# Optimization experiments

Measured on AMD Instinct MI355X. Metric: run time of the kernel, lower is better.

Reference implementation:

```python
import jax, jax.numpy as jnp
import numpy as np

N = 50000      # nodes
E = 1600000    # edges (before self loops)
F = 128        # input_dim
H = 4          # num_heads
D = 32         # hidden_dim (per head)
B = 16         # graphs in batch
NEG_SLOPE = 0.2  # PyG GATv2Conv default negative_slope


def setup_inputs() -> dict:
    key = jax.random.key(0)
    ks = jax.random.split(key, 8)
    x = jax.random.normal(ks[0], (N, F), dtype=jnp.float32)
    edge_index = jax.random.randint(ks[1], (2, E), 0, N, dtype=jnp.int32)
    batch = jnp.sort(jax.random.randint(ks[2], (N,), 0, B, dtype=jnp.int32))
    s = 0.05
    W_l = jax.random.normal(ks[3], (F, H * D), dtype=jnp.float32) * s
    b_l = jnp.zeros((H * D,), dtype=jnp.float32)
    W_r = jax.random.normal(ks[4], (F, H * D), dtype=jnp.float32) * s
    b_r = jnp.zeros((H * D,), dtype=jnp.float32)
    att = jax.random.normal(ks[5], (H, D), dtype=jnp.float32) * s
    bias = jnp.zeros((H * D,), dtype=jnp.float32)
    return {"x": x, "edge_index": edge_index, "batch": batch,
            "W_l": W_l, "b_l": b_l, "W_r": W_r, "b_r": b_r,
            "att": att, "bias": bias}


def reference(x, edge_index, batch, W_l, b_l, W_r, b_r, att, bias):
    n = x.shape[0]
    # PyG GATv2Conv adds self loops by default
    loops = jnp.arange(n, dtype=edge_index.dtype)
    src = jnp.concatenate([edge_index[0], loops])  # message source j
    dst = jnp.concatenate([edge_index[1], loops])  # message target i

    xl = (x @ W_l + b_l).reshape(n, H, D)  # source transform
    xr = (x @ W_r + b_r).reshape(n, H, D)  # target transform

    # per-edge GATv2 attention logits: a^T LeakyReLU(xl_j + xr_i)
    m = xl[src] + xr[dst]                                   # [E+N, H, D]
    e = jnp.sum(jax.nn.leaky_relu(m, NEG_SLOPE) * att, -1)  # [E+N, H]

    # softmax over incoming edges of each destination node
    e_max = jax.ops.segment_max(e, dst, num_segments=n)
    ex = jnp.exp(e - e_max[dst])
    den = jax.ops.segment_sum(ex, dst, num_segments=n)
    alpha = ex / den[dst]                                   # [E+N, H]

    # weighted scatter-sum aggregation of source features
    out = jax.ops.segment_sum(alpha[..., None] * xl[src], dst, num_segments=n)
    out = out.reshape(n, H * D) + bias                      # concat heads + bias
    out = jax.nn.relu(out)

    # global max pool over nodes of each graph
    pooled = jax.ops.segment_max(out, batch, num_segments=B)
    pooled = jnp.where(jnp.isfinite(pooled), pooled, 0.0)   # guard empty graphs
    return pooled
```

## Files before the change

### kernel.cpp

```cpp
#include <hip/hip_runtime.h>

#define NN 50000
#define NE 1600000
#define FDIM 128
#define CDIM 128
#define NGRAPH 16
#define SLOPE 0.2f
#define CSTRIDE 96
#define BINSH 7
#define NBIN 391
#define EPB 6400
#define NB1 250
#define EPT 25
#define CAP 5120
#define POOL_NODES 64
#define POOL_NB ((NN + POOL_NODES - 1) / POOL_NODES)
#define TNB 782

__device__ __forceinline__ unsigned short f2bf(float f) {
    unsigned u = __float_as_uint(f);
    return (unsigned short)((u + 0x7FFFu + ((u >> 16) & 1u)) >> 16);
}
__device__ __forceinline__ unsigned packbf(float a, float b) {
    return (unsigned)f2bf(a) | ((unsigned)f2bf(b) << 16);
}
#define BFLO(u) __uint_as_float((u) << 16)
#define BFHI(u) __uint_as_float((u) & 0xffff0000u)

typedef __attribute__((ext_vector_type(8))) short short8;
typedef __attribute__((ext_vector_type(4))) float f32x4;
union FragU { uint4 u; short8 s; };

__global__ __launch_bounds__(256) void k_init(float* __restrict__ out,
                                              int* __restrict__ gbin_cnt) {
    int i = blockIdx.x * 256 + threadIdx.x;
    if (i < NGRAPH * CDIM) out[i] = 0.f;
    if (i < NBIN) gbin_cnt[i] = 0;
}

__global__ __launch_bounds__(256) void k_front(
    const float* __restrict__ x,
    const float* __restrict__ Wl, const float* __restrict__ bl,
    const float* __restrict__ Wr, const float* __restrict__ br,
    const int* __restrict__ src, const int* __restrict__ dst,
    int* __restrict__ gbin_cnt, unsigned* __restrict__ gstage,
    unsigned short* __restrict__ xlh, float* __restrict__ xr) {
    __shared__ __align__(16) char shraw[32768];
    const int tid = threadIdx.x;

    if (blockIdx.x < NB1) {
        int* bcnt = (int*)shraw;
        int* boff = bcnt + NBIN;
        int* gb   = boff + NBIN;
        int* sc   = gb + NBIN;
        unsigned* st = (unsigned*)(sc + 256);
        const int t  = tid;
        const int e0 = blockIdx.x * EPB;

        for (int b = t; b < NBIN; b += 256) bcnt[b] = 0;
        __syncthreads();

        unsigned sd[EPT]; int bn[EPT]; int pl[EPT];
#pragma unroll
        for (int k = 0; k < EPT; k++) {
            int e = e0 + k * 256 + t;
            int s = src[e], d = dst[e];
            bn[k] = d >> BINSH;
            sd[k] = (unsigned)s | ((unsigned)(d & 127) << 16)
                                | ((unsigned)bn[k] << 23);
            pl[k] = atomicAdd(&bcnt[bn[k]], 1);
        }
        __syncthreads();

        int c0 = (2*t     < NBIN) ? bcnt[2*t]     : 0;
        int c1 = (2*t + 1 < NBIN) ? bcnt[2*t + 1] : 0;
        int v  = c0 + c1;
        sc[t] = v; __syncthreads();
        for (int off = 1; off < 256; off <<= 1) {
            int add = (t >= off) ? sc[t - off] : 0;
            __syncthreads();
            sc[t] += add;
            __syncthreads();
        }
        int base = sc[t] - v;
        if (2*t     < NBIN) boff[2*t]     = base;
        if (2*t + 1 < NBIN) boff[2*t + 1] = base + c0;
        __syncthreads();

        for (int b = t; b < NBIN; b += 256) {
            int c = bcnt[b];
            gb[b] = (c > 0) ? atomicAdd(&gbin_cnt[b], c) : 0;
        }
#pragma unroll
        for (int k = 0; k < EPT; k++) st[boff[bn[k]] + pl[k]] = sd[k];
        __syncthreads();

        for (int idx = t; idx < EPB; idx += 256) {
            unsigned w = st[idx];
            int b = w >> 23;
            int p = gb[b] + (idx - boff[b]);
            if (p < CAP) gstage[(size_t)b * CAP + p] = w;
        }
    } else {
        uint4* wfrag = (uint4*)shraw;
        const int bid   = blockIdx.x - NB1;
        const int wv    = tid >> 6;
        const int lane  = tid & 63;
        const int quad  = lane >> 4;
        const int col   = lane & 15;
        const int node0 = bid * 64;
        const int nodeA = node0 + wv * 16 + col;
        const bool aval = nodeA < NN;

        FragU afrag[4];
#pragma unroll
        for (int kq = 0; kq < 4; kq++) {
            float4 lo = make_float4(0.f,0.f,0.f,0.f), hi = lo;
            if (aval) {
                const float* ap = &x[(size_t)nodeA * FDIM + kq * 32 + quad * 8];
                lo = *(const float4*)ap;
                hi = *(const float4*)(ap + 4);
            }
            afrag[kq].u.x = packbf(lo.x, lo.y);
            afrag[kq].u.y = packbf(lo.z, lo.w);
            afrag[kq].u.z = packbf(hi.x, hi.y);
            afrag[kq].u.w = packbf(hi.z, hi.w);
        }

        const int myrow0 = node0 + wv * 16 + quad * 4;

        for (int mat = 0; mat < 2; mat++) {
            const float* W  = mat ? Wr : Wl;
            const float* bb = mat ? br : bl;
            __syncthreads();
            for (int i = 0; i < 8; i++) {
                int C = i * 256 + tid;
                int ccol = C & 15, cq = (C >> 4) & 3, ckq = (C >> 6) & 3, cnt_ = C >> 8;
                const float* wp = &W[(size_t)(ckq * 32 + cq * 8) * CDIM + cnt_ * 16 + ccol];
                uint4 u;
                u.x = packbf(wp[0],        wp[CDIM]);
                u.y = packbf(wp[2*CDIM],   wp[3*CDIM]);
                u.z = packbf(wp[4*CDIM],   wp[5*CDIM]);
                u.w = packbf(wp[6*CDIM],   wp[7*CDIM]);
                wfrag[C] = u;
            }
            __syncthreads();

#pragma unroll
            for (int nt = 0; nt < 8; nt++) {
                f32x4 acc = {0.f, 0.f, 0.f, 0.f};
#pragma unroll
                for (int kq = 0; kq < 4; kq++) {
                    FragU bfr;
                    bfr.u = wfrag[(nt * 4 + kq) * 64 + lane];
                    acc = __builtin_amdgcn_mfma_f32_16x16x32_bf16(
                              afrag[kq].s, bfr.s, acc, 0, 0, 0);
                }
                int ch = nt * 16 + col;
                float bv = bb[ch];
                if (mat == 0) {
#pragma unroll
                    for (int r = 0; r < 4; r++) {
                        int node = myrow0 + r;
                        if (node < NN)
                            xlh[(size_t)node * CDIM + ch] = f2bf(acc[r] + bv);
                    }
                } else {
#pragma unroll
                    for (int r = 0; r < 4; r++) {
                        int node = myrow0 + r;
                        if (node < NN)
                            xr[(size_t)node * CDIM + ch] = acc[r] + bv;
                    }
                }
            }
        }
    }
}

__global__ __launch_bounds__(512) void k_csr(
    const int* __restrict__ gbin_cnt, const unsigned* __restrict__ gstage,
    int* __restrict__ cnt, unsigned short* __restrict__ colp) {
    __shared__ int nfill[128];
    __shared__ unsigned short crow[128 * CSTRIDE];
    const int bin = blockIdx.x;
    const int t   = threadIdx.x;
    const int n0  = bin << BINSH;
    const int nb  = min(128, NN - n0);
    const int m   = min(gbin_cnt[bin], CAP);

    if (t < 128) nfill[t] = 0;
    __syncthreads();

    unsigned w[10];
    bool     ok[10];
#pragma unroll
    for (int k = 0; k < 10; k++) {
        int i = k * 512 + t;
        ok[k] = i < m;
        if (ok[k]) w[k] = gstage[(size_t)bin * CAP + i];
    }
#pragma unroll
    for (int k = 0; k < 10; k++) {
        if (ok[k]) {
            int dl = (w[k] >> 16) & 127;
            int p  = atomicAdd(&nfill[dl], 1);
            if (p < CSTRIDE - 1)
                crow[dl * CSTRIDE + p] = (unsigned short)(w[k] & 0xFFFF);
        }
    }
    __syncthreads();

    if (t < nb) {
        int c = min(nfill[t], CSTRIDE - 1);
        crow[t * CSTRIDE + c] = (unsigned short)(n0 + t);
        cnt[n0 + t] = c + 1;
    }
    __syncthreads();

    unsigned* gout = (unsigned*)colp + (size_t)bin * (128 * CSTRIDE / 2);
    const unsigned* cin = (const unsigned*)crow;
    for (int idx = t; idx < 128 * CSTRIDE / 2; idx += 512) gout[idx] = cin[idx];
}

__device__ __forceinline__ void edge_body(
    const unsigned short* __restrict__ xlh, int j, int ch0,
    const float4& rx0, const float4& rx1,
    const float4& p0, const float4& p1,
    const float4& q0, const float4& q1,
    float& s, float* acc) {
    uint4 q = *(const uint4*)&xlh[(size_t)j * CDIM + ch0];
    float4 v0 = make_float4(BFLO(q.x), BFHI(q.x), BFLO(q.y), BFHI(q.y));
    float4 v1 = make_float4(BFLO(q.z), BFHI(q.z), BFLO(q.w), BFHI(q.w));
    float t0, d = 0.f;
    t0 = v0.x + rx0.x; d = fmaf(t0, p0.x, d); d = fmaf(fabsf(t0), q0.x, d);
    t0 = v0.y + rx0.y; d = fmaf(t0, p0.y, d); d = fmaf(fabsf(t0), q0.y, d);
    t0 = v0.z + rx0.z; d = fmaf(t0, p0.z, d); d = fmaf(fabsf(t0), q0.z, d);
    t0 = v0.w + rx0.w; d = fmaf(t0, p0.w, d); d = fmaf(fabsf(t0), q0.w, d);
    t0 = v1.x + rx1.x; d = fmaf(t0, p1.x, d); d = fmaf(fabsf(t0), q1.x, d);
    t0 = v1.y + rx1.y; d = fmaf(t0, p1.y, d); d = fmaf(fabsf(t0), q1.y, d);
    t0 = v1.z + rx1.z; d = fmaf(t0, p1.z, d); d = fmaf(fabsf(t0), q1.z, d);
    t0 = v1.w + rx1.w; d = fmaf(t0, p1.w, d); d = fmaf(fabsf(t0), q1.w, d);
    d += __shfl_xor(d, 1);
    d += __shfl_xor(d, 2);
    float w = __expf(d);
    s += w;
    acc[0] = fmaf(w, v0.x, acc[0]);
    acc[1] = fmaf(w, v0.y, acc[1]);
    acc[2] = fmaf(w, v0.z, acc[2]);
    acc[3] = fmaf(w, v0.w, acc[3]);
    acc[4] = fmaf(w, v1.x, acc[4]);
    acc[5] = fmaf(w, v1.y, acc[5]);
    acc[6] = fmaf(w, v1.z, acc[6]);
    acc[7] = fmaf(w, v1.w, acc[7]);
}

__global__ __launch_bounds__(256) void k_aggregate(
    const unsigned short* __restrict__ xlh, const float* __restrict__ xr,
    const float* __restrict__ att, const float* __restrict__ bias,
    const int* __restrict__ cnt, const unsigned short* __restrict__ colp,
    float* __restrict__ nodeout) {
    const int wave = blockIdx.x * 4 + (threadIdx.x >> 6);
    const int lane = threadIdx.x & 63;
    const int i     = wave;
    const size_t start = (size_t)i * CSTRIDE;
    const int deg   = cnt[i];
    const int grp   = lane >> 4;
    const int ch0   = (lane & 15) * 8;

    int cj0 = (int)colp[start + lane];
    int cj1 = 0;
    if (deg > 64) cj1 = (int)colp[start + 64 + lane];

    const float4 rx0 = *(const float4*)&xr[(size_t)i * CDIM + ch0];
    const float4 rx1 = *(const float4*)&xr[(size_t)i * CDIM + ch0 + 4];
    const float4 aa0 = *(const float4*)&att[ch0];
    const float4 aa1 = *(const float4*)&att[ch0 + 4];
    const float4 p0 = make_float4(0.6f*aa0.x, 0.6f*aa0.y, 0.6f*aa0.z, 0.6f*aa0.w);
    const float4 p1 = make_float4(0.6f*aa1.x, 0.6f*aa1.y, 0.6f*aa1.z, 0.6f*aa1.w);
    const float4 q0 = make_float4(0.4f*aa0.x, 0.4f*aa0.y, 0.4f*aa0.z, 0.4f*aa0.w);
    const float4 q1 = make_float4(0.4f*aa1.x, 0.4f*aa1.y, 0.4f*aa1.z, 0.4f*aa1.w);

    float s = 0.f;
    float acc[8];
#pragma unroll
    for (int k = 0; k < 8; k++) acc[k] = 0.f;

    const int full = deg >> 2;
    const int f0   = full < 16 ? full : 16;
#pragma unroll 2
    for (int t = 0; t < f0; t++) {
        int j = __shfl(cj0, t * 4 + grp);
        edge_body(xlh, j, ch0, rx0, rx1, p0, p1, q0, q1, s, acc);
    }
    for (int t = 16; t < full; t++) {
        int j = __shfl(cj1, t * 4 + grp - 64);
        edge_body(xlh, j, ch0, rx0, rx1, p0, p1, q0, q1, s, acc);
    }
    int e  = full * 4 + grp;
    int jt = (e < 64) ? __shfl(cj0, e) : __shfl(cj1, (e - 64) & 63);
    if (e < deg)
        edge_body(xlh, jt, ch0, rx0, rx1, p0, p1, q0, q1, s, acc);

#pragma unroll
    for (int dist = 16; dist <= 32; dist <<= 1) {
        s += __shfl_xor(s, dist);
#pragma unroll
        for (int k = 0; k < 8; k++) acc[k] += __shfl_xor(acc[k], dist);
    }

    if (grp == 0) {
        float inv = 1.f / s;
        float4 o0, o1;
        const float4 b0 = *(const float4*)&bias[ch0];
        const float4 b1 = *(const float4*)&bias[ch0 + 4];
        o0.x = fmaxf(fmaf(acc[0], inv, b0.x), 0.f);
        o0.y = fmaxf(fmaf(acc[1], inv, b0.y), 0.f);
        o0.z = fmaxf(fmaf(acc[2], inv, b0.z), 0.f);
        o0.w = fmaxf(fmaf(acc[3], inv, b0.w), 0.f);
        o1.x = fmaxf(fmaf(acc[4], inv, b1.x), 0.f);
        o1.y = fmaxf(fmaf(acc[5], inv, b1.y), 0.f);
        o1.z = fmaxf(fmaf(acc[6], inv, b1.z), 0.f);
        o1.w = fmaxf(fmaf(acc[7], inv, b1.w), 0.f);
        float* op = &nodeout[(size_t)i * CDIM + ch0];
        *(float4*)op       = o0;
        *(float4*)(op + 4) = o1;
    }
}

__global__ __launch_bounds__(256) void k_pool(
    const float* __restrict__ nodeout, const int* __restrict__ batch,
    float* __restrict__ out) {
    const int tid  = threadIdx.x;
    const int c4   = (tid & 31) * 4;
    const int nl   = tid >> 5;
    const int base = blockIdx.x * POOL_NODES;
    float4 mx = make_float4(0.f, 0.f, 0.f, 0.f);
    int cur = -1;
#pragma unroll
    for (int k = 0; k < POOL_NODES / 8; k++) {
        int node = base + k * 8 + nl;
        if (node >= NN) break;
        int g = batch[node];
        if (g != cur) {
            if (cur >= 0) {
                int* op = (int*)&out[cur * CDIM + c4];
                if (mx.x > 0.f) atomicMax(op,     __float_as_int(mx.x));
                if (mx.y > 0.f) atomicMax(op + 1, __float_as_int(mx.y));
                if (mx.z > 0.f) atomicMax(op + 2, __float_as_int(mx.z));
                if (mx.w > 0.f) atomicMax(op + 3, __float_as_int(mx.w));
            }
            cur = g;
            mx = make_float4(0.f, 0.f, 0.f, 0.f);
        }
        float4 v = *(const float4*)&nodeout[(size_t)node * CDIM + c4];
        mx.x = fmaxf(mx.x, v.x);
        mx.y = fmaxf(mx.y, v.y);
        mx.z = fmaxf(mx.z, v.z);
        mx.w = fmaxf(mx.w, v.w);
    }
    if (cur >= 0) {
        int* op = (int*)&out[cur * CDIM + c4];
        if (mx.x > 0.f) atomicMax(op,     __float_as_int(mx.x));
        if (mx.y > 0.f) atomicMax(op + 1, __float_as_int(mx.y));
        if (mx.z > 0.f) atomicMax(op + 2, __float_as_int(mx.z));
        if (mx.w > 0.f) atomicMax(op + 3, __float_as_int(mx.w));
    }
}

extern "C" void kernel_launch(void* const* d_in, const int* in_sizes, int n_in,
                              void* d_out, int out_size, void* d_ws, size_t ws_size,
                              hipStream_t stream) {
    const float* x     = (const float*)d_in[0];
    const int*   ei    = (const int*)d_in[1];
    const int*   batch = (const int*)d_in[2];
    const float* Wl    = (const float*)d_in[3];
    const float* bl    = (const float*)d_in[4];
    const float* Wr    = (const float*)d_in[5];
    const float* br    = (const float*)d_in[6];
    const float* att   = (const float*)d_in[7];
    const float* bias  = (const float*)d_in[8];
    float* out = (float*)d_out;

    char* w = (char*)d_ws;
    float*          xr       = (float*)w;          w += (size_t)NN * CDIM * 4;
    float*          nodeout  = (float*)w;          w += (size_t)NN * CDIM * 4;
    unsigned short* xlh      = (unsigned short*)w; w += (size_t)NN * CDIM * 2;
    int*            cnt      = (int*)w;            w += (size_t)NN * 4;
    unsigned short* colp     = (unsigned short*)w; w += (size_t)NBIN * 128 * CSTRIDE * 2;
    unsigned*       gstage   = (unsigned*)w;       w += (size_t)NBIN * CAP * 4;
    int*            gbin_cnt = (int*)w;            w += (size_t)NBIN * 4;

    const int* src = ei;
    const int* dst = ei + NE;

    k_init<<<10, 256, 0, stream>>>(out, gbin_cnt);
    k_front<<<NB1 + TNB, 256, 0, stream>>>(x, Wl, bl, Wr, br,
                                           src, dst, gbin_cnt, gstage, xlh, xr);
    k_csr<<<NBIN, 512, 0, stream>>>(gbin_cnt, gstage, cnt, colp);
    k_aggregate<<<NN / 4, 256, 0, stream>>>(xlh, xr, att, bias,
                                            cnt, colp, nodeout);
    k_pool<<<POOL_NB, 256, 0, stream>>>(nodeout, batch, out);
}
```

Baseline: 233.0 us.

## Use fp16 packed math for edge logits and fuse max-pool into aggregation

Stores both xl and xr as fp16 instead of bf16 and fp32. The per-edge logit is computed with packed half adds, a max-based LeakyReLU and fdot2 dot products, replacing the scalar fp32 FMA chain. The separate pooling kernel and the nodeout buffer are removed: each node's result goes straight into the per-graph output through atomicMax, guarded by a pre-read. This cuts memory traffic and per-edge ALU work, at the cost of fp16 precision loss and more global atomics on the 16x128 output.

```diff
diff --git a/kernel.cpp b/kernel.cpp
--- a/kernel.cpp
+++ b/kernel.cpp
@@ -13,8 +13,6 @@
 #define NB1 250
 #define EPT 25
 #define CAP 5120
-#define POOL_NODES 64
-#define POOL_NB ((NN + POOL_NODES - 1) / POOL_NODES)
 #define TNB 782
 
 __device__ __forceinline__ unsigned short f2bf(float f) {
@@ -24,12 +22,17 @@
 __device__ __forceinline__ unsigned packbf(float a, float b) {
     return (unsigned)f2bf(a) | ((unsigned)f2bf(b) << 16);
 }
-#define BFLO(u) __uint_as_float((u) << 16)
-#define BFHI(u) __uint_as_float((u) & 0xffff0000u)
+__device__ __forceinline__ unsigned short f2h(float f) {
+    union { _Float16 h; unsigned short u; } c;
+    c.h = (_Float16)f;
+    return c.u;
+}
 
 typedef __attribute__((ext_vector_type(8))) short short8;
 typedef __attribute__((ext_vector_type(4))) float f32x4;
+typedef _Float16 h2 __attribute__((ext_vector_type(2)));
 union FragU { uint4 u; short8 s; };
+union HU    { uint4 u; h2 h[4]; };
 
 __global__ __launch_bounds__(256) void k_init(float* __restrict__ out,
                                               int* __restrict__ gbin_cnt) {
@@ -44,7 +47,7 @@
     const float* __restrict__ Wr, const float* __restrict__ br,
     const int* __restrict__ src, const int* __restrict__ dst,
     int* __restrict__ gbin_cnt, unsigned* __restrict__ gstage,
-    unsigned short* __restrict__ xlh, float* __restrict__ xr) {
+    unsigned short* __restrict__ xlh, unsigned short* __restrict__ xrh) {
     __shared__ __align__(16) char shraw[32768];
     const int tid = threadIdx.x;
 
@@ -132,6 +135,7 @@
         for (int mat = 0; mat < 2; mat++) {
             const float* W  = mat ? Wr : Wl;
             const float* bb = mat ? br : bl;
+            unsigned short* dsto = mat ? xrh : xlh;
             __syncthreads();
             for (int i = 0; i < 8; i++) {
                 int C = i * 256 + tid;
@@ -158,20 +162,11 @@
                 }
                 int ch = nt * 16 + col;
                 float bv = bb[ch];
-                if (mat == 0) {
-#pragma unroll
-                    for (int r = 0; r < 4; r++) {
-                        int node = myrow0 + r;
-                        if (node < NN)
-                            xlh[(size_t)node * CDIM + ch] = f2bf(acc[r] + bv);
-                    }
-                } else {
-#pragma unroll
-                    for (int r = 0; r < 4; r++) {
-                        int node = myrow0 + r;
-                        if (node < NN)
-                            xr[(size_t)node * CDIM + ch] = acc[r] + bv;
-                    }
+#pragma unroll
+                for (int r = 0; r < 4; r++) {
+                    int node = myrow0 + r;
+                    if (node < NN)
+                        dsto[(size_t)node * CDIM + ch] = f2h(acc[r] + bv);
                 }
             }
         }
@@ -224,42 +219,40 @@
 }
 
 __device__ __forceinline__ void edge_body(
-    const unsigned short* __restrict__ xlh, int j, int ch0,
-    const float4& rx0, const float4& rx1,
-    const float4& p0, const float4& p1,
-    const float4& q0, const float4& q1,
-    float& s, float* acc) {
-    uint4 q = *(const uint4*)&xlh[(size_t)j * CDIM + ch0];
-    float4 v0 = make_float4(BFLO(q.x), BFHI(q.x), BFLO(q.y), BFHI(q.y));
-    float4 v1 = make_float4(BFLO(q.z), BFHI(q.z), BFLO(q.w), BFHI(q.w));
-    float t0, d = 0.f;
-    t0 = v0.x + rx0.x; d = fmaf(t0, p0.x, d); d = fmaf(fabsf(t0), q0.x, d);
-    t0 = v0.y + rx0.y; d = fmaf(t0, p0.y, d); d = fmaf(fabsf(t0), q0.y, d);
-    t0 = v0.z + rx0.z; d = fmaf(t0, p0.z, d); d = fmaf(fabsf(t0), q0.z, d);
-    t0 = v0.w + rx0.w; d = fmaf(t0, p0.w, d); d = fmaf(fabsf(t0), q0.w, d);
-    t0 = v1.x + rx1.x; d = fmaf(t0, p1.x, d); d = fmaf(fabsf(t0), q1.x, d);
-    t0 = v1.y + rx1.y; d = fmaf(t0, p1.y, d); d = fmaf(fabsf(t0), q1.y, d);
-    t0 = v1.z + rx1.z; d = fmaf(t0, p1.z, d); d = fmaf(fabsf(t0), q1.z, d);
-    t0 = v1.w + rx1.w; d = fmaf(t0, p1.w, d); d = fmaf(fabsf(t0), q1.w, d);
+    const char* __restrict__ xlb, unsigned chb, int j,
+    const h2* __restrict__ rx, const h2* __restrict__ ah,
+    float& s, float* __restrict__ acc) {
+    HU q;
+    q.u = *(const uint4*)(xlb + (((unsigned)j << 8) | chb));
+    const h2 c02 = {(_Float16)SLOPE, (_Float16)SLOPE};
+    float d = 0.f;
+#pragma unroll
+    for (int k = 0; k < 4; k++) {
+        h2 t  = q.h[k] + rx[k];
+        h2 lk = __builtin_elementwise_max(t, t * c02);
+#if __has_builtin(__builtin_amdgcn_fdot2)
+        d = __builtin_amdgcn_fdot2(lk, ah[k], d, false);
+#else
+        d = fmaf((float)lk.x, (float)ah[k].x, d);
+        d = fmaf((float)lk.y, (float)ah[k].y, d);
+#endif
+    }
     d += __shfl_xor(d, 1);
     d += __shfl_xor(d, 2);
     float w = __expf(d);
     s += w;
-    acc[0] = fmaf(w, v0.x, acc[0]);
-    acc[1] = fmaf(w, v0.y, acc[1]);
-    acc[2] = fmaf(w, v0.z, acc[2]);
-    acc[3] = fmaf(w, v0.w, acc[3]);
-    acc[4] = fmaf(w, v1.x, acc[4]);
-    acc[5] = fmaf(w, v1.y, acc[5]);
-    acc[6] = fmaf(w, v1.z, acc[6]);
-    acc[7] = fmaf(w, v1.w, acc[7]);
+#pragma unroll
+    for (int k = 0; k < 4; k++) {
+        acc[2*k]   = fmaf(w, (float)q.h[k].x, acc[2*k]);
+        acc[2*k+1] = fmaf(w, (float)q.h[k].y, acc[2*k+1]);
+    }
 }
 
 __global__ __launch_bounds__(256) void k_aggregate(
-    const unsigned short* __restrict__ xlh, const float* __restrict__ xr,
+    const unsigned short* __restrict__ xlh, const unsigned short* __restrict__ xrh,
     const float* __restrict__ att, const float* __restrict__ bias,
     const int* __restrict__ cnt, const unsigned short* __restrict__ colp,
-    float* __restrict__ nodeout) {
+    const int* __restrict__ batch, float* __restrict__ out) {
     const int wave = blockIdx.x * 4 + (threadIdx.x >> 6);
     const int lane = threadIdx.x & 63;
     const int i     = wave;
@@ -267,19 +260,22 @@
     const int deg   = cnt[i];
     const int grp   = lane >> 4;
     const int ch0   = (lane & 15) * 8;
+    const unsigned chb = (unsigned)(ch0 * 2);
+    const char* xlb = (const char*)xlh;
 
     int cj0 = (int)colp[start + lane];
     int cj1 = 0;
     if (deg > 64) cj1 = (int)colp[start + 64 + lane];
 
-    const float4 rx0 = *(const float4*)&xr[(size_t)i * CDIM + ch0];
-    const float4 rx1 = *(const float4*)&xr[(size_t)i * CDIM + ch0 + 4];
+    HU rxu;
+    rxu.u = *(const uint4*)&xrh[(size_t)i * CDIM + ch0];
     const float4 aa0 = *(const float4*)&att[ch0];
     const float4 aa1 = *(const float4*)&att[ch0 + 4];
-    const float4 p0 = make_float4(0.6f*aa0.x, 0.6f*aa0.y, 0.6f*aa0.z, 0.6f*aa0.w);
-    const float4 p1 = make_float4(0.6f*aa1.x, 0.6f*aa1.y, 0.6f*aa1.z, 0.6f*aa1.w);
-    const float4 q0 = make_float4(0.4f*aa0.x, 0.4f*aa0.y, 0.4f*aa0.z, 0.4f*aa0.w);
-    const float4 q1 = make_float4(0.4f*aa1.x, 0.4f*aa1.y, 0.4f*aa1.z, 0.4f*aa1.w);
+    h2 ah[4];
+    ah[0] = h2{(_Float16)aa0.x, (_Float16)aa0.y};
+    ah[1] = h2{(_Float16)aa0.z, (_Float16)aa0.w};
+    ah[2] = h2{(_Float16)aa1.x, (_Float16)aa1.y};
+    ah[3] = h2{(_Float16)aa1.z, (_Float16)aa1.w};
 
     float s = 0.f;
     float acc[8];
@@ -291,16 +287,16 @@
 #pragma unroll 2
     for (int t = 0; t < f0; t++) {
         int j = __shfl(cj0, t * 4 + grp);
-        edge_body(xlh, j, ch0, rx0, rx1, p0, p1, q0, q1, s, acc);
+        edge_body(xlb, chb, j, rxu.h, ah, s, acc);
     }
     for (int t = 16; t < full; t++) {
         int j = __shfl(cj1, t * 4 + grp - 64);
-        edge_body(xlh, j, ch0, rx0, rx1, p0, p1, q0, q1, s, acc);
+        edge_body(xlb, chb, j, rxu.h, ah, s, acc);
     }
     int e  = full * 4 + grp;
     int jt = (e < 64) ? __shfl(cj0, e) : __shfl(cj1, (e - 64) & 63);
     if (e < deg)
-        edge_body(xlh, jt, ch0, rx0, rx1, p0, p1, q0, q1, s, acc);
+        edge_body(xlb, chb, jt, rxu.h, ah, s, acc);
 
 #pragma unroll
     for (int dist = 16; dist <= 32; dist <<= 1) {
@@ -311,60 +307,30 @@
 
     if (grp == 0) {
         float inv = 1.f / s;
-        float4 o0, o1;
         const float4 b0 = *(const float4*)&bias[ch0];
         const float4 b1 = *(const float4*)&bias[ch0 + 4];
-        o0.x = fmaxf(fmaf(acc[0], inv, b0.x), 0.f);
-        o0.y = fmaxf(fmaf(acc[1], inv, b0.y), 0.f);
-        o0.z = fmaxf(fmaf(acc[2], inv, b0.z), 0.f);
-        o0.w = fmaxf(fmaf(acc[3], inv, b0.w), 0.f);
-        o1.x = fmaxf(fmaf(acc[4], inv, b1.x), 0.f);
-        o1.y = fmaxf(fmaf(acc[5], inv, b1.y), 0.f);
-        o1.z = fmaxf(fmaf(acc[6], inv, b1.z), 0.f);
-        o1.w = fmaxf(fmaf(acc[7], inv, b1.w), 0.f);
-        float* op = &nodeout[(size_t)i * CDIM + ch0];
-        *(float4*)op       = o0;
-        *(float4*)(op + 4) = o1;
-    }
-}
-
-__global__ __launch_bounds__(256) void k_pool(
-    const float* __restrict__ nodeout, const int* __restrict__ batch,
-    float* __restrict__ out) {
-    const int tid  = threadIdx.x;
-    const int c4   = (tid & 31) * 4;
-    const int nl   = tid >> 5;
-    const int base = blockIdx.x * POOL_NODES;
-    float4 mx = make_float4(0.f, 0.f, 0.f, 0.f);
-    int cur = -1;
-#pragma unroll
-    for (int k = 0; k < POOL_NODES / 8; k++) {
-        int node = base + k * 8 + nl;
-        if (node >= NN) break;
-        int g = batch[node];
-        if (g != cur) {
-            if (cur >= 0) {
-                int* op = (int*)&out[cur * CDIM + c4];
-                if (mx.x > 0.f) atomicMax(op,     __float_as_int(mx.x));
-                if (mx.y > 0.f) atomicMax(op + 1, __float_as_int(mx.y));
-                if (mx.z > 0.f) atomicMax(op + 2, __float_as_int(mx.z));
-                if (mx.w > 0.f) atomicMax(op + 3, __float_as_int(mx.w));
-            }
-            cur = g;
-            mx = make_float4(0.f, 0.f, 0.f, 0.f);
-        }
-        float4 v = *(const float4*)&nodeout[(size_t)node * CDIM + c4];
-        mx.x = fmaxf(mx.x, v.x);
-        mx.y = fmaxf(mx.y, v.y);
-        mx.z = fmaxf(mx.z, v.z);
-        mx.w = fmaxf(mx.w, v.w);
-    }
-    if (cur >= 0) {
-        int* op = (int*)&out[cur * CDIM + c4];
-        if (mx.x > 0.f) atomicMax(op,     __float_as_int(mx.x));
-        if (mx.y > 0.f) atomicMax(op + 1, __float_as_int(mx.y));
-        if (mx.z > 0.f) atomicMax(op + 2, __float_as_int(mx.z));
-        if (mx.w > 0.f) atomicMax(op + 3, __float_as_int(mx.w));
+        float o[8];
+        o[0] = fmaxf(fmaf(acc[0], inv, b0.x), 0.f);
+        o[1] = fmaxf(fmaf(acc[1], inv, b0.y), 0.f);
+        o[2] = fmaxf(fmaf(acc[2], inv, b0.z), 0.f);
+        o[3] = fmaxf(fmaf(acc[3], inv, b0.w), 0.f);
+        o[4] = fmaxf(fmaf(acc[4], inv, b1.x), 0.f);
+        o[5] = fmaxf(fmaf(acc[5], inv, b1.y), 0.f);
+        o[6] = fmaxf(fmaf(acc[6], inv, b1.z), 0.f);
+        o[7] = fmaxf(fmaf(acc[7], inv, b1.w), 0.f);
+
+        const int g = batch[i];
+        float* op = &out[g * CDIM + ch0];
+        float4 c0 = *(const float4*)op;
+        float4 c1 = *(const float4*)(op + 4);
+        if (o[0] > c0.x) atomicMax((int*)op + 0, __float_as_int(o[0]));
+        if (o[1] > c0.y) atomicMax((int*)op + 1, __float_as_int(o[1]));
+        if (o[2] > c0.z) atomicMax((int*)op + 2, __float_as_int(o[2]));
+        if (o[3] > c0.w) atomicMax((int*)op + 3, __float_as_int(o[3]));
+        if (o[4] > c1.x) atomicMax((int*)op + 4, __float_as_int(o[4]));
+        if (o[5] > c1.y) atomicMax((int*)op + 5, __float_as_int(o[5]));
+        if (o[6] > c1.z) atomicMax((int*)op + 6, __float_as_int(o[6]));
+        if (o[7] > c1.w) atomicMax((int*)op + 7, __float_as_int(o[7]));
     }
 }
 
@@ -383,9 +349,8 @@
     float* out = (float*)d_out;
 
     char* w = (char*)d_ws;
-    float*          xr       = (float*)w;          w += (size_t)NN * CDIM * 4;
-    float*          nodeout  = (float*)w;          w += (size_t)NN * CDIM * 4;
     unsigned short* xlh      = (unsigned short*)w; w += (size_t)NN * CDIM * 2;
+    unsigned short* xrh      = (unsigned short*)w; w += (size_t)NN * CDIM * 2;
     int*            cnt      = (int*)w;            w += (size_t)NN * 4;
     unsigned short* colp     = (unsigned short*)w; w += (size_t)NBIN * 128 * CSTRIDE * 2;
     unsigned*       gstage   = (unsigned*)w;       w += (size_t)NBIN * CAP * 4;
@@ -396,9 +361,8 @@
 
     k_init<<<10, 256, 0, stream>>>(out, gbin_cnt);
     k_front<<<NB1 + TNB, 256, 0, stream>>>(x, Wl, bl, Wr, br,
-                                           src, dst, gbin_cnt, gstage, xlh, xr);
+                                           src, dst, gbin_cnt, gstage, xlh, xrh);
     k_csr<<<NBIN, 512, 0, stream>>>(gbin_cnt, gstage, cnt, colp);
-    k_aggregate<<<NN / 4, 256, 0, stream>>>(xlh, xr, att, bias,
-                                            cnt, colp, nodeout);
-    k_pool<<<POOL_NB, 256, 0, stream>>>(nodeout, batch, out);
-}
+    k_aggregate<<<NN / 4, 256, 0, stream>>>(xlh, xrh, att, bias,
+                                            cnt, colp, batch, out);
+}
```

Result: slower. 532.1 us (+128.3%).
